# Performance work log

Hardware: AMD Instinct MI355X
Metric: run time of the kernel (lower is better)

Reference implementation:

```python
import jax, jax.numpy as jnp
import numpy as np
from jax import lax

ACT_BIT = 8
WEIGHT_BIT = 8


def _sym_scale(amin, amax, n):
    # symmetric quantization scale = max(|min|,|max|)/ (2^(b-1)-1)
    return jnp.maximum(jnp.maximum(jnp.abs(amin), jnp.abs(amax)), 1e-8) / n


def _fake_quant(x, scale, n):
    # clamp(round(x/scale), -(n+1), n) * scale  (integer-simulated, then dequant)
    q = jnp.clip(jnp.round(x / scale), -(n + 1.0), n) * scale
    return q


def setup_inputs() -> dict:
    key = jax.random.key(0)
    k1, k2, k3 = jax.random.split(key, 3)
    x = jax.random.normal(k1, (8, 2048, 32, 32), dtype=jnp.float32)
    weight = jax.random.normal(k2, (256, 2048, 1, 1), dtype=jnp.float32) * 0.02
    bias = jax.random.normal(k3, (256,), dtype=jnp.float32) * 0.02
    return {"x": x, "weight": weight, "bias": bias}


def reference(x, weight, bias):
    n_a = float(2 ** (ACT_BIT - 1) - 1)
    n_w = float(2 ** (WEIGHT_BIT - 1) - 1)

    # ---- QuantAct: global symmetric activation fake-quant ----
    s_a = _sym_scale(x.min(), x.max(), n_a)  # scalar
    x_q = _fake_quant(x, s_a, n_a)           # [B, Cin, H, W]

    # ---- QuantConv2d: per-output-channel symmetric weight quant ----
    co = weight.shape[0]
    w_flat = weight.reshape(co, -1)
    s_w = _sym_scale(w_flat.min(axis=1), w_flat.max(axis=1), n_w)  # [Co]
    w_q = _fake_quant(weight, s_w[:, None, None, None], n_w)

    # bias quantized at the combined scale s_a * s_w (integer-simulated bias)
    s_b = s_a * s_w
    b_q = jnp.round(bias / s_b) * s_b

    # 1x1 conv, NCHW / OIHW
    out = lax.conv_general_dilated(
        x_q, w_q, window_strides=(1, 1), padding="VALID",
        dimension_numbers=("NCHW", "OIHW", "NCHW"))
    out = out + b_q[None, :, None, None]
    return out
```

## Files before the change

### kernel.cpp

```cpp
#include <hip/hip_runtime.h>
#include <hip/hip_bf16.h>

typedef __attribute__((ext_vector_type(8))) short bf16x8;
typedef __attribute__((ext_vector_type(4))) float f32x4;

#define CO    256
#define CI    2048
#define BATCH 8
#define HW    1024
#define NTOT  (BATCH * CI * HW)

#define BK    32
#define BHW   32
#define LDSA  40
#define LDSB  40

static __device__ __forceinline__ float fabs4max(const float4 v) {
  return fmaxf(fmaxf(fabsf(v.x), fabsf(v.y)), fmaxf(fabsf(v.z), fabsf(v.w)));
}

static __device__ __forceinline__ short f32_to_bf16_bits(float f) {
  return (short)(__float_as_uint(f) >> 16);
}

static __device__ __forceinline__ short quant1(float v, float inv_s) {
  return f32_to_bf16_bits(fminf(fmaxf(rintf(v * inv_s), -128.0f), 127.0f));
}

__global__ __launch_bounds__(256) void absmax_kernel(const float* __restrict__ x,
                                                     unsigned int* __restrict__ absbits,
                                                     long long n4) {
  long long i = (long long)blockIdx.x * blockDim.x + threadIdx.x;
  const long long stride = (long long)gridDim.x * blockDim.x;
  const float4* x4 = (const float4*)x;
  float m0 = 0.0f, m1 = 0.0f;
  for (; i + stride < n4; i += 2 * stride) {
    m0 = fmaxf(m0, fabs4max(x4[i]));
    m1 = fmaxf(m1, fabs4max(x4[i + stride]));
  }
  if (i < n4) m0 = fmaxf(m0, fabs4max(x4[i]));
  float m = fmaxf(m0, m1);
#pragma unroll
  for (int off = 32; off; off >>= 1) m = fmaxf(m, __shfl_xor(m, off));
  __shared__ float red[4];
  if ((threadIdx.x & 63) == 0) red[threadIdx.x >> 6] = m;
  __syncthreads();
  if (threadIdx.x == 0) {
    m = fmaxf(fmaxf(red[0], red[1]), fmaxf(red[2], red[3]));
    atomicMax(absbits, __float_as_uint(m));
  }
}

__global__ __launch_bounds__(256) void wquant_kernel(const float* __restrict__ w,
                                                     const float* __restrict__ bias,
                                                     const unsigned int* __restrict__ absbits,
                                                     short* __restrict__ qw,
                                                     float* __restrict__ alpha,
                                                     float* __restrict__ beta) {
  const int co = blockIdx.x;
  const int t = threadIdx.x;
  const float* row = w + (size_t)co * CI;
  const float4 v0 = ((const float4*)row)[t * 2];
  const float4 v1 = ((const float4*)row)[t * 2 + 1];
  float m = fmaxf(fabs4max(v0), fabs4max(v1));
#pragma unroll
  for (int off = 32; off; off >>= 1) m = fmaxf(m, __shfl_xor(m, off));
  __shared__ float red[4];
  __shared__ float s_sw;
  if ((t & 63) == 0) red[t >> 6] = m;
  __syncthreads();
  if (t == 0) {
    const float mm = fmaxf(fmaxf(red[0], red[1]), fmaxf(red[2], red[3]));
    s_sw = fmaxf(mm, 1e-8f) / 127.0f;
  }
  __syncthreads();
  const float sw = s_sw;

  const float vals[8] = {v0.x, v0.y, v0.z, v0.w, v1.x, v1.y, v1.z, v1.w};
  bf16x8 qv;
#pragma unroll
  for (int j = 0; j < 8; ++j) {
    const float q = fminf(fmaxf(rintf(vals[j] / sw), -128.0f), 127.0f);
    qv[j] = f32_to_bf16_bits(q);
  }
  *(bf16x8*)(qw + (size_t)co * CI + t * 8) = qv;

  if (t == 0) {
    const float sa = fmaxf(__uint_as_float(*absbits), 1e-8f) / 127.0f;
    const float a = sa * sw;
    alpha[co] = a;
    beta[co] = rintf(bias[co] / a) * a;
  }
}

__global__ __launch_bounds__(512) void gemm_kernel(const float* __restrict__ x,
                                                   const short* __restrict__ qw,
                                                   const float* __restrict__ alpha,
                                                   const float* __restrict__ beta,
                                                   const unsigned int* __restrict__ absbits,
                                                   float* __restrict__ out) {
  __shared__ short As[CO * LDSA];
  __shared__ short Bs[BHW * LDSB];

  const int hwt = blockIdx.x & 31;
  const int b = blockIdx.x >> 5;
  const int hw0 = hwt * BHW;

  const float sa = fmaxf(__uint_as_float(*absbits), 1e-8f) / 127.0f;
  const float inv_sa = 1.0f / sa;

  const int t = threadIdx.x;
  const int lane = t & 63;
  const int w = t >> 6;
  const int wco = (w & 3) * 64;
  const int whw = (w >> 2) * 16;
  const int lr = lane & 15;
  const int kg = lane >> 4;

  const int arow = t >> 1;
  const int ak = (t & 1) * 16;
  const int bk = t >> 4;
  const int bhw = (t & 15) * 2;

  const short* ap0 = qw + (size_t)arow * CI + ak;
  const float* xp0 = x + ((size_t)b * CI + bk) * HW + hw0 + bhw;

  f32x4 acc[4] = {};

  bf16x8 av0 = *(const bf16x8*)(ap0);
  bf16x8 av1 = *(const bf16x8*)(ap0 + 8);
  float2 xv = *(const float2*)(xp0);

  for (int k0 = 0; k0 < CI; k0 += BK) {
    __syncthreads();
    *(bf16x8*)&As[arow * LDSA + ak] = av0;
    *(bf16x8*)&As[arow * LDSA + ak + 8] = av1;
    Bs[bhw * LDSB + bk] = quant1(xv.x, inv_sa);
    Bs[(bhw + 1) * LDSB + bk] = quant1(xv.y, inv_sa);

    const int kn = (k0 + BK) & (CI - 1);
    av0 = *(const bf16x8*)(ap0 + kn);
    av1 = *(const bf16x8*)(ap0 + kn + 8);
    xv = *(const float2*)(xp0 + (size_t)kn * HW);

    __syncthreads();

    const bf16x8 aF = *(const bf16x8*)&Bs[(whw + lr) * LDSB + kg * 8];
#pragma unroll
    for (int n = 0; n < 4; ++n) {
      const bf16x8 bF = *(const bf16x8*)&As[(wco + n * 16 + lr) * LDSA + kg * 8];
      acc[n] = __builtin_amdgcn_mfma_f32_16x16x32_bf16(aF, bF, acc[n], 0, 0, 0);
    }
  }

  const int hwo = hw0 + whw + kg * 4;
#pragma unroll
  for (int n = 0; n < 4; ++n) {
    const int co = wco + n * 16 + lr;
    const float af = alpha[co];
    const float bf = beta[co];
    float4 v;
    v.x = acc[n][0] * af + bf;
    v.y = acc[n][1] * af + bf;
    v.z = acc[n][2] * af + bf;
    v.w = acc[n][3] * af + bf;
    *(float4*)(out + ((size_t)(b * CO + co)) * HW + hwo) = v;
  }
}

extern "C" void kernel_launch(void* const* d_in, const int* in_sizes, int n_in,
                              void* d_out, int out_size, void* d_ws, size_t ws_size,
                              hipStream_t stream) {
  const float* x    = (const float*)d_in[0];
  const float* wgt  = (const float*)d_in[1];
  const float* bias = (const float*)d_in[2];
  float* out = (float*)d_out;

  unsigned int* absbits = (unsigned int*)d_ws;
  short* qw    = (short*)((char*)d_ws + 256);
  float* alpha = (float*)((char*)d_ws + 256 + (size_t)CO * CI * 2);
  float* beta  = alpha + CO;

  hipMemsetAsync(d_ws, 0, 4, stream);
  absmax_kernel<<<2048, 256, 0, stream>>>(x, absbits, (long long)(NTOT / 4));
  wquant_kernel<<<CO, 256, 0, stream>>>(wgt, bias, absbits, qw, alpha, beta);
  gemm_kernel<<<BATCH * 32, 512, 0, stream>>>(x, qw, alpha, beta, absbits, out);
}
```

Measured before the change: 153.0 us.

## Retile GEMM to 16-wide HW tiles with BK=64 and XOR-swizzled LDS

The GEMM tile is reshaped from 32 HW columns x 32 K with 512 threads to 16 HW columns x 64 K with 256 threads. The grid doubles to 512 blocks so more of the GPU's compute units get work. LDS padding is replaced with an XOR swizzle to avoid bank conflicts, and each thread now loads a float4 of activations and a full 64-element weight row per step. The absmax reduction loop is also unrolled four ways. In exchange, each block re-reads the whole weight tile for fewer output columns, which raises L2 traffic and register pressure.

After: 182.4 us. +19.2%, slower.

```diff
diff --git a/kernel.cpp b/kernel.cpp
--- a/kernel.cpp
+++ b/kernel.cpp
@@ -10,10 +10,9 @@
 #define HW    1024
 #define NTOT  (BATCH * CI * HW)
 
-#define BK    32
-#define BHW   32
-#define LDSA  40
-#define LDSB  40
+#define BK    64
+#define BHW   16
+#define LDA   64
 
 static __device__ __forceinline__ float fabs4max(const float4 v) {
   return fmaxf(fmaxf(fabsf(v.x), fabsf(v.y)), fmaxf(fabsf(v.z), fabsf(v.w)));
@@ -33,13 +32,15 @@
   long long i = (long long)blockIdx.x * blockDim.x + threadIdx.x;
   const long long stride = (long long)gridDim.x * blockDim.x;
   const float4* x4 = (const float4*)x;
-  float m0 = 0.0f, m1 = 0.0f;
-  for (; i + stride < n4; i += 2 * stride) {
+  float m0 = 0.0f, m1 = 0.0f, m2 = 0.0f, m3 = 0.0f;
+  for (; i + 3 * stride < n4; i += 4 * stride) {
     m0 = fmaxf(m0, fabs4max(x4[i]));
     m1 = fmaxf(m1, fabs4max(x4[i + stride]));
-  }
-  if (i < n4) m0 = fmaxf(m0, fabs4max(x4[i]));
-  float m = fmaxf(m0, m1);
+    m2 = fmaxf(m2, fabs4max(x4[i + 2 * stride]));
+    m3 = fmaxf(m3, fabs4max(x4[i + 3 * stride]));
+  }
+  for (; i < n4; i += stride) m0 = fmaxf(m0, fabs4max(x4[i]));
+  float m = fmaxf(fmaxf(m0, m1), fmaxf(m2, m3));
 #pragma unroll
   for (int off = 32; off; off >>= 1) m = fmaxf(m, __shfl_xor(m, off));
   __shared__ float red[4];
@@ -93,17 +94,17 @@
   }
 }
 
-__global__ __launch_bounds__(512) void gemm_kernel(const float* __restrict__ x,
+__global__ __launch_bounds__(256) void gemm_kernel(const float* __restrict__ x,
                                                    const short* __restrict__ qw,
                                                    const float* __restrict__ alpha,
                                                    const float* __restrict__ beta,
                                                    const unsigned int* __restrict__ absbits,
                                                    float* __restrict__ out) {
-  __shared__ short As[CO * LDSA];
-  __shared__ short Bs[BHW * LDSB];
-
-  const int hwt = blockIdx.x & 31;
-  const int b = blockIdx.x >> 5;
+  __shared__ short As[CO * LDA];
+  __shared__ short Bs[BHW * LDA];
+
+  const int hwt = blockIdx.x & 63;
+  const int b = blockIdx.x >> 6;
   const int hw0 = hwt * BHW;
 
   const float sa = fmaxf(__uint_as_float(*absbits), 1e-8f) / 127.0f;
@@ -112,48 +113,62 @@
   const int t = threadIdx.x;
   const int lane = t & 63;
   const int w = t >> 6;
-  const int wco = (w & 3) * 64;
-  const int whw = (w >> 2) * 16;
+  const int wco = w * 64;
   const int lr = lane & 15;
   const int kg = lane >> 4;
-
-  const int arow = t >> 1;
-  const int ak = (t & 1) * 16;
-  const int bk = t >> 4;
-  const int bhw = (t & 15) * 2;
-
-  const short* ap0 = qw + (size_t)arow * CI + ak;
+  const int rsw = lr & 7;
+
+  const int arow = t;
+  const int asw = arow & 7;
+  const int bk = t >> 2;
+  const int bhw = (t & 3) * 4;
+
+  const short* ap0 = qw + (size_t)arow * CI;
   const float* xp0 = x + ((size_t)b * CI + bk) * HW + hw0 + bhw;
 
   f32x4 acc[4] = {};
 
-  bf16x8 av0 = *(const bf16x8*)(ap0);
-  bf16x8 av1 = *(const bf16x8*)(ap0 + 8);
-  float2 xv = *(const float2*)(xp0);
+  bf16x8 av[8];
+  float4 xv;
+#pragma unroll
+  for (int s = 0; s < 8; ++s) av[s] = *(const bf16x8*)(ap0 + s * 8);
+  xv = *(const float4*)(xp0);
 
   for (int k0 = 0; k0 < CI; k0 += BK) {
     __syncthreads();
-    *(bf16x8*)&As[arow * LDSA + ak] = av0;
-    *(bf16x8*)&As[arow * LDSA + ak + 8] = av1;
-    Bs[bhw * LDSB + bk] = quant1(xv.x, inv_sa);
-    Bs[(bhw + 1) * LDSB + bk] = quant1(xv.y, inv_sa);
+#pragma unroll
+    for (int s = 0; s < 8; ++s)
+      *(bf16x8*)&As[arow * LDA + ((s ^ asw) << 3)] = av[s];
+    {
+      const int sl = bk >> 3, kq = bk & 7;
+      const float f[4] = {xv.x, xv.y, xv.z, xv.w};
+#pragma unroll
+      for (int j = 0; j < 4; ++j) {
+        const int row = bhw + j;
+        Bs[row * LDA + ((sl ^ (row & 7)) << 3) + kq] = quant1(f[j], inv_sa);
+      }
+    }
 
     const int kn = (k0 + BK) & (CI - 1);
-    av0 = *(const bf16x8*)(ap0 + kn);
-    av1 = *(const bf16x8*)(ap0 + kn + 8);
-    xv = *(const float2*)(xp0 + (size_t)kn * HW);
+#pragma unroll
+    for (int s = 0; s < 8; ++s) av[s] = *(const bf16x8*)(ap0 + kn + s * 8);
+    xv = *(const float4*)(xp0 + (size_t)kn * HW);
 
     __syncthreads();
 
-    const bf16x8 aF = *(const bf16x8*)&Bs[(whw + lr) * LDSB + kg * 8];
-#pragma unroll
-    for (int n = 0; n < 4; ++n) {
-      const bf16x8 bF = *(const bf16x8*)&As[(wco + n * 16 + lr) * LDSA + kg * 8];
-      acc[n] = __builtin_amdgcn_mfma_f32_16x16x32_bf16(aF, bF, acc[n], 0, 0, 0);
+#pragma unroll
+    for (int h = 0; h < 2; ++h) {
+      const int ph = ((h * 4 + kg) ^ rsw) << 3;
+      const bf16x8 aF = *(const bf16x8*)&Bs[lr * LDA + ph];
+#pragma unroll
+      for (int n = 0; n < 4; ++n) {
+        const bf16x8 bF = *(const bf16x8*)&As[(wco + n * 16 + lr) * LDA + ph];
+        acc[n] = __builtin_amdgcn_mfma_f32_16x16x32_bf16(aF, bF, acc[n], 0, 0, 0);
+      }
     }
   }
 
-  const int hwo = hw0 + whw + kg * 4;
+  const int hwo = hw0 + kg * 4;
 #pragma unroll
   for (int n = 0; n < 4; ++n) {
     const int co = wco + n * 16 + lr;
@@ -184,5 +199,5 @@
   hipMemsetAsync(d_ws, 0, 4, stream);
   absmax_kernel<<<2048, 256, 0, stream>>>(x, absbits, (long long)(NTOT / 4));
   wquant_kernel<<<CO, 256, 0, stream>>>(wgt, bias, absbits, qw, alpha, beta);
-  gemm_kernel<<<BATCH * 32, 512, 0, stream>>>(x, qw, alpha, beta, absbits, out);
-}
+  gemm_kernel<<<BATCH * 64, 256, 0, stream>>>(x, qw, alpha, beta, absbits, out);
+}
```
